# Optimization experiments

Measured on AMD Instinct MI355X. Metric: run time of the kernel, lower is better.

The kernel has to match this reference:

```python
import jax, jax.numpy as jnp
import numpy as np

L2_LAMDA = 0.001
RECONS_LAMDA = 0.2
LB_TH = 0.01
B, N, D = 32, 2048, 256


def setup_inputs() -> dict:
    key = jax.random.key(0)
    k1, k2, k3, k4 = jax.random.split(key, 4)
    cur = jax.random.normal(k1, (B, N, D), jnp.float32)
    pre = jax.random.normal(k2, (B, N, D), jnp.float32)
    lim_r = float(np.sqrt(6.0 / (D + D)))  # xavier_uniform bound
    r_proj = jax.random.uniform(k3, (D, D), jnp.float32, -lim_r, lim_r)
    lim_i = float(np.sqrt(6.0 / (N + N)))
    incidence_m = jax.random.uniform(k4, (N, N), jnp.float32, -lim_i, lim_i)
    return {"cur": cur, "pre": pre, "r_proj": r_proj, "incidence_m": incidence_m}


def reference(cur, pre, r_proj, incidence_m):
    # torch forward detaches cur/pre
    cur = jax.lax.stop_gradient(cur)
    pre = jax.lax.stop_gradient(pre)
    # clamp(min=lb_th) then zero where not (> lb_th)  ==  keep original where > lb_th else 0
    W = jnp.where(incidence_m > LB_TH, incidence_m, 0.0)          # (N, N)
    proj = jnp.einsum('bnd,de->bne', cur, r_proj)                 # (B, N, D)
    neigh = jnp.einsum('nm,bmd->bnd', W, pre)                     # (B, N, D)
    recon_err = jnp.sqrt(jnp.sum((proj - neigh) ** 2, axis=-1))   # (B, N)
    # torch: max(sum(abs(row[None,:]), dim=0)) == max-abs of the masked row
    l1 = jnp.max(jnp.abs(W), axis=1)                              # (N,)
    l2 = jnp.sqrt(jnp.sum(W ** 2, axis=1))                        # (N,)
    per_node = recon_err * RECONS_LAMDA + l1[None, :] + L2_LAMDA * l2[None, :]
    loss = jnp.sum(per_node, axis=1, keepdims=True)               # (B, 1)
    return loss, incidence_m
```

## Files before the change

### kernel.cpp

```cpp
#include <hip/hip_runtime.h>


typedef __attribute__((ext_vector_type(8))) short bf16x8;
typedef __attribute__((ext_vector_type(8))) unsigned short ushort8;
typedef __attribute__((ext_vector_type(16))) float f32x16;

__device__ __forceinline__ unsigned short f2bf(float f) {
    union { float f; unsigned u; } x; x.f = f;
    unsigned r = x.u + 0x7fffu + ((x.u >> 16) & 1u);
    return (unsigned short)(r >> 16);
}

#define GLL16(g, l)                                                         \
    __builtin_amdgcn_global_load_lds(                                       \
        (const __attribute__((address_space(1))) void*)(g),                 \
        (__attribute__((address_space(3))) void*)(l), 16, 0, 0)

__device__ __forceinline__ void transpose_64x64(
    const float* __restrict__ src, unsigned short* __restrict__ dst,
    int R, int C, int r0, int c0, unsigned short* __restrict__ tile) {
    const int t = threadIdx.x;
    const int fr = t >> 4, fc = (t & 15) * 4;
#pragma unroll
    for (int it = 0; it < 4; ++it) {
        int m = fr + it * 16;
        float4 v = *(const float4*)(src + (size_t)(r0 + m) * C + c0 + fc);
        tile[(fc + 0) * 68 + m] = f2bf(v.x);
        tile[(fc + 1) * 68 + m] = f2bf(v.y);
        tile[(fc + 2) * 68 + m] = f2bf(v.z);
        tile[(fc + 3) * 68 + m] = f2bf(v.w);
    }
    __syncthreads();
    const int d = t >> 2, m0 = (t & 3) * 16;
    unsigned short v[16];
#pragma unroll
    for (int j = 0; j < 4; ++j)
        *(ushort4*)(v + j * 4) = *(const ushort4*)(tile + d * 68 + m0 + j * 4);
    unsigned short* dp = dst + (size_t)(c0 + d) * R + r0 + m0;
    ushort8 p0, p1;
#pragma unroll
    for (int j = 0; j < 8; ++j) { p0[j] = v[j]; p1[j] = v[8 + j]; }
    *(ushort8*)(dp) = p0;
    *(ushort8*)(dp + 8) = p1;
}

__global__ __launch_bounds__(256) void prep_inc(
    const float* __restrict__ inc, float* __restrict__ out_inc,
    unsigned short* __restrict__ Wneg, float* __restrict__ crow) {
    __shared__ float smax[4], ssum[4];
    const int row = blockIdx.x;
    const int t = threadIdx.x;
    const float4* src = (const float4*)(inc + (size_t)row * 2048);
    float4* dst = (float4*)(out_inc + (size_t)row * 2048);
    ushort4* wp = (ushort4*)(Wneg + (size_t)row * 2048);
    float lmax = 0.f, ss = 0.f;
#pragma unroll
    for (int it = 0; it < 2; ++it) {
        int i = it * 256 + t;
        float4 v = src[i];
        dst[i] = v;
        float w0 = v.x > 0.01f ? v.x : 0.f;
        float w1 = v.y > 0.01f ? v.y : 0.f;
        float w2 = v.z > 0.01f ? v.z : 0.f;
        float w3 = v.w > 0.01f ? v.w : 0.f;
        ushort4 p;
        p.x = f2bf(-w0); p.y = f2bf(-w1); p.z = f2bf(-w2); p.w = f2bf(-w3);
        wp[i] = p;
        lmax = fmaxf(lmax, fmaxf(fmaxf(w0, w1), fmaxf(w2, w3)));
        ss += w0 * w0 + w1 * w1 + w2 * w2 + w3 * w3;
    }
#pragma unroll
    for (int off = 32; off; off >>= 1) {
        lmax = fmaxf(lmax, __shfl_down(lmax, off));
        ss += __shfl_down(ss, off);
    }
    int wv = t >> 6, ln = t & 63;
    if (ln == 0) { smax[wv] = lmax; ssum[wv] = ss; }
    __syncthreads();
    if (t == 0) {
        float m = fmaxf(fmaxf(smax[0], smax[1]), fmaxf(smax[2], smax[3]));
        float s = ssum[0] + ssum[1] + ssum[2] + ssum[3];
        crow[row] = m + 0.001f * sqrtf(s);
    }
}

__global__ __launch_bounds__(256) void prep_tr(
    const float* __restrict__ pre, unsigned short* __restrict__ preT,
    const float* __restrict__ r_proj, unsigned short* __restrict__ rprojT) {
    __shared__ unsigned short tile[64 * 68];
    const int bid = blockIdx.x;
    if (bid < 4096) {
        const int b = bid >> 7;
        const int mt = (bid & 127) >> 2;
        const int dt = bid & 3;
        transpose_64x64(pre + (size_t)b * 524288, preT + (size_t)b * 524288,
                        2048, 256, mt * 64, dt * 64, tile);
    } else {
        const int tt = bid - 4096;
        transpose_64x64(r_proj, rprojT, 256, 256, (tt >> 2) * 64, (tt & 3) * 64,
                        tile);
    }
}

__global__ __launch_bounds__(1024) void gemm_diff(
    const unsigned short* __restrict__ Wneg,
    const float* __restrict__ cur,
    const unsigned short* __restrict__ preT,
    const unsigned short* __restrict__ rprojT,
    float* __restrict__ Ssq)
{
    const int n0 = blockIdx.x * 256;
    const int b  = blockIdx.y;

    __shared__ unsigned short Al[2 * 256 * 64];
    __shared__ unsigned short Bl[2 * 256 * 64];
    __shared__ float ssq[256];

    const int tid  = threadIdx.x;
    const int w    = tid >> 6;
    const int lane = tid & 63;
    const int l32  = lane & 31;
    const int half = lane >> 5;
    const int wm   = w >> 2;
    const int wn   = w & 3;
    const int w8   = w * 8;
    const int grow  = lane >> 3;
    const int gbyte = ((lane & 7) ^ grow) * 16;
    const int sw    = (l32 & 7) * 8;

    if (tid < 256) ssq[tid] = 0.f;

    f32x16 acc[2][2] = {};

    const float*          curB = cur  + (size_t)b * 2048 * 256;
    const unsigned short* preB = preT + (size_t)b * 256 * 2048;
    const unsigned short* An   = Wneg + (size_t)n0 * 2048;

#define STAGE_TILE(AP, BP, K0)                                                 \
    {                                                                          \
        _Pragma("unroll") for (int pass = 0; pass < 2; ++pass) {               \
            const int rowb = pass * 128 + w8;                                  \
            GLL16((const char*)(An + (size_t)(rowb + grow) * 2048 + (K0)) + gbyte, \
                  (char*)(AP) + rowb * 128);                                   \
        }                                                                      \
        _Pragma("unroll") for (int pass = 0; pass < 2; ++pass) {               \
            const int rowb = pass * 128 + w8;                                  \
            GLL16((const char*)(preB + (size_t)(rowb + grow) * 2048 + (K0)) + gbyte, \
                  (char*)(BP) + rowb * 128);                                   \
        }                                                                      \
    }

#define KS_LOOP(Ac, Bc)                                                        \
    _Pragma("unroll") for (int ks = 0; ks < 4; ++ks) {                         \
        const int ck = (ks * 2 + half) * 8;                                    \
        bf16x8 af[2], bfr[2];                                                  \
        _Pragma("unroll") for (int mi = 0; mi < 2; ++mi)                       \
            af[mi] = *(const bf16x8*)((Ac) + (wm * 64 + mi * 32 + l32) * 64 +  \
                                      (ck ^ sw));                              \
        _Pragma("unroll") for (int ni = 0; ni < 2; ++ni)                       \
            bfr[ni] = *(const bf16x8*)((Bc) + (wn * 64 + ni * 32 + l32) * 64 + \
                                       (ck ^ sw));                             \
        _Pragma("unroll") for (int mi = 0; mi < 2; ++mi)                       \
        _Pragma("unroll") for (int ni = 0; ni < 2; ++ni)                       \
            acc[mi][ni] = __builtin_amdgcn_mfma_f32_32x32x16_bf16(             \
                af[mi], bfr[ni], acc[mi][ni], 0, 0, 0);                        \
    }

    STAGE_TILE(Al, Bl, 0);

    for (int t = 0; t < 32; ++t) {
        unsigned short* Ac = Al + (t & 1) * 16384;
        unsigned short* Bc = Bl + (t & 1) * 16384;
        unsigned short* Anx = Al + ((t & 1) ^ 1) * 16384;
        unsigned short* Bnx = Bl + ((t & 1) ^ 1) * 16384;

        asm volatile("s_waitcnt vmcnt(0)" ::: "memory");
        asm volatile("s_barrier" ::: "memory");
        if (t < 31) { STAGE_TILE(Anx, Bnx, (t + 1) * 64); }
        KS_LOOP(Ac, Bc)
    }

    for (int kt = 32; kt < 36; ++kt) {
        __syncthreads();
        const int kk = (kt - 32) * 64;
        const int row = tid >> 2;
        const int q   = tid & 3;
#pragma unroll
        for (int i = 0; i < 4; ++i) {
            const int k4 = q * 4 + i;
            float4 v = *(const float4*)(curB + (size_t)(n0 + row) * 256 + kk + k4 * 4);
            ushort4 p;
            p.x = f2bf(v.x); p.y = f2bf(v.y); p.z = f2bf(v.z); p.w = f2bf(v.w);
            const int pos = ((k4 >> 1) ^ (row & 7)) * 8 + (k4 & 1) * 4;
            *(ushort4*)(Al + row * 64 + pos) = p;
        }
#pragma unroll
        for (int pass = 0; pass < 2; ++pass) {
            const int rowb = pass * 128 + w8;
            GLL16((const char*)(rprojT + (size_t)(rowb + grow) * 256 + kk) + gbyte,
                  (char*)Bl + rowb * 128);
        }
        __syncthreads();
        KS_LOOP(Al, Bl)
    }
    __syncthreads();

#pragma unroll
    for (int mi = 0; mi < 2; ++mi)
#pragma unroll
        for (int reg = 0; reg < 16; ++reg) {
            float s = 0.f;
#pragma unroll
            for (int ni = 0; ni < 2; ++ni) {
                float v = acc[mi][ni][reg];
                s += v * v;
            }
            s += __shfl_xor(s, 1);
            s += __shfl_xor(s, 2);
            s += __shfl_xor(s, 4);
            s += __shfl_xor(s, 8);
            s += __shfl_xor(s, 16);
            if (l32 == 0) {
                const int row = wm * 64 + mi * 32 +
                                (reg & 3) + 8 * (reg >> 2) + 4 * half;
                atomicAdd(&ssq[row], s);
            }
        }
    __syncthreads();
    if (tid < 256)
        Ssq[(size_t)b * 2048 + n0 + tid] = sqrtf(ssq[tid]);
}

__global__ void finalize(const float* __restrict__ Ssq,
                         const float* __restrict__ crow,
                         float* __restrict__ out) {
    const int b = blockIdx.x;
    float s1 = 0.f, s2 = 0.f;
    for (int i = threadIdx.x; i < 2048; i += 256) {
        s1 += Ssq[(size_t)b * 2048 + i];
        s2 += crow[i];
    }
#pragma unroll
    for (int off = 32; off; off >>= 1) {
        s1 += __shfl_down(s1, off);
        s2 += __shfl_down(s2, off);
    }
    __shared__ float sm1[4], sm2[4];
    int wv = threadIdx.x >> 6, ln = threadIdx.x & 63;
    if (ln == 0) { sm1[wv] = s1; sm2[wv] = s2; }
    __syncthreads();
    if (threadIdx.x == 0)
        out[b] = 0.2f * (sm1[0] + sm1[1] + sm1[2] + sm1[3])
               + (sm2[0] + sm2[1] + sm2[2] + sm2[3]);
}

extern "C" void kernel_launch(void* const* d_in, const int* in_sizes, int n_in,
                              void* d_out, int out_size, void* d_ws, size_t ws_size,
                              hipStream_t stream) {
    const float* cur    = (const float*)d_in[0];
    const float* pre    = (const float*)d_in[1];
    const float* r_proj = (const float*)d_in[2];
    const float* inc    = (const float*)d_in[3];
    float* out = (float*)d_out;

    char* ws = (char*)d_ws;
    unsigned short* Wneg   = (unsigned short*)(ws + 0);
    unsigned short* preT   = (unsigned short*)(ws + 8388608);
    unsigned short* rprojT = (unsigned short*)(ws + 41943040);
    float*          Sbuf   = (float*)(ws + 42074112);
    float*          crow   = (float*)(ws + 42336256);

    prep_inc<<<2048, 256, 0, stream>>>(inc, out + 32, Wneg, crow);
    prep_tr<<<4112, 256, 0, stream>>>(pre, preT, r_proj, rprojT);
    gemm_diff<<<dim3(8, 32), 1024, 0, stream>>>(Wneg, cur, preT, rprojT, Sbuf);
    finalize<<<32, 256, 0, stream>>>(Sbuf, crow, out);
}
```

Measured before the change: 254.6 us.

## Pre-convert cur to bf16 and use 4-stage K32 async pipeline in gemm

Moves the fp32-to-bf16 conversion of cur into the prep kernel so the projection phase of the GEMM can use the same async global-to-LDS loads as the main phase. The GEMM loop is restructured into a uniform 72-step pipeline with 32-wide K tiles and a 4-deep LDS ring buffer, prefetching three tiles ahead using partial vmcnt waits instead of a full drain each step. This aims to hide memory latency and remove the synchronous tail loop, at the cost of an extra 32 MB write/read of cur in bf16 and more barriers per K.

```diff
diff --git a/kernel.cpp b/kernel.cpp
--- a/kernel.cpp
+++ b/kernel.cpp
@@ -86,25 +86,37 @@
 
 __global__ __launch_bounds__(256) void prep_tr(
     const float* __restrict__ pre, unsigned short* __restrict__ preT,
-    const float* __restrict__ r_proj, unsigned short* __restrict__ rprojT) {
+    const float* __restrict__ r_proj, unsigned short* __restrict__ rprojT,
+    const float* __restrict__ cur, unsigned short* __restrict__ curbf) {
     __shared__ unsigned short tile[64 * 68];
     const int bid = blockIdx.x;
+    const int t = threadIdx.x;
     if (bid < 4096) {
         const int b = bid >> 7;
         const int mt = (bid & 127) >> 2;
         const int dt = bid & 3;
         transpose_64x64(pre + (size_t)b * 524288, preT + (size_t)b * 524288,
                         2048, 256, mt * 64, dt * 64, tile);
-    } else {
+    } else if (bid < 4112) {
         const int tt = bid - 4096;
         transpose_64x64(r_proj, rprojT, 256, 256, (tt >> 2) * 64, (tt & 3) * 64,
                         tile);
+    } else {
+        const size_t base = (size_t)(bid - 4112) * 8192;
+#pragma unroll
+        for (int i = 0; i < 8; ++i) {
+            size_t idx = base + (size_t)(i * 256 + t) * 4;
+            float4 v = *(const float4*)(cur + idx);
+            ushort4 p;
+            p.x = f2bf(v.x); p.y = f2bf(v.y); p.z = f2bf(v.z); p.w = f2bf(v.w);
+            *(ushort4*)(curbf + idx) = p;
+        }
     }
 }
 
 __global__ __launch_bounds__(1024) void gemm_diff(
     const unsigned short* __restrict__ Wneg,
-    const float* __restrict__ cur,
+    const unsigned short* __restrict__ curbf,
     const unsigned short* __restrict__ preT,
     const unsigned short* __restrict__ rprojT,
     float* __restrict__ Ssq)
@@ -112,8 +124,8 @@
     const int n0 = blockIdx.x * 256;
     const int b  = blockIdx.y;
 
-    __shared__ unsigned short Al[2 * 256 * 64];
-    __shared__ unsigned short Bl[2 * 256 * 64];
+    __shared__ unsigned short Ab[4 * 256 * 32];
+    __shared__ unsigned short Bb[4 * 256 * 32];
     __shared__ float ssq[256];
 
     const int tid  = threadIdx.x;
@@ -123,85 +135,65 @@
     const int half = lane >> 5;
     const int wm   = w >> 2;
     const int wn   = w & 3;
-    const int w8   = w * 8;
-    const int grow  = lane >> 3;
-    const int gbyte = ((lane & 7) ^ grow) * 16;
-    const int sw    = (l32 & 7) * 8;
+    const int w16  = w * 16;
+    const int srow  = lane >> 2;
+    const int sbyte = ((lane & 3) ^ ((lane >> 3) & 3)) * 16;
+    const int q2    = (l32 >> 1) & 3;
 
     if (tid < 256) ssq[tid] = 0.f;
 
     f32x16 acc[2][2] = {};
 
-    const float*          curB = cur  + (size_t)b * 2048 * 256;
+    const unsigned short* curA = curbf + (size_t)b * 2048 * 256 + (size_t)n0 * 256;
     const unsigned short* preB = preT + (size_t)b * 256 * 2048;
     const unsigned short* An   = Wneg + (size_t)n0 * 2048;
 
-#define STAGE_TILE(AP, BP, K0)                                                 \
+#define STAGEPAIR(T, AB, AS, BB, BS, KK)                                       \
     {                                                                          \
-        _Pragma("unroll") for (int pass = 0; pass < 2; ++pass) {               \
-            const int rowb = pass * 128 + w8;                                  \
-            GLL16((const char*)(An + (size_t)(rowb + grow) * 2048 + (K0)) + gbyte, \
-                  (char*)(AP) + rowb * 128);                                   \
-        }                                                                      \
-        _Pragma("unroll") for (int pass = 0; pass < 2; ++pass) {               \
-            const int rowb = pass * 128 + w8;                                  \
-            GLL16((const char*)(preB + (size_t)(rowb + grow) * 2048 + (K0)) + gbyte, \
-                  (char*)(BP) + rowb * 128);                                   \
-        }                                                                      \
-    }
-
-#define KS_LOOP(Ac, Bc)                                                        \
-    _Pragma("unroll") for (int ks = 0; ks < 4; ++ks) {                         \
-        const int ck = (ks * 2 + half) * 8;                                    \
-        bf16x8 af[2], bfr[2];                                                  \
-        _Pragma("unroll") for (int mi = 0; mi < 2; ++mi)                       \
-            af[mi] = *(const bf16x8*)((Ac) + (wm * 64 + mi * 32 + l32) * 64 +  \
-                                      (ck ^ sw));                              \
-        _Pragma("unroll") for (int ni = 0; ni < 2; ++ni)                       \
-            bfr[ni] = *(const bf16x8*)((Bc) + (wn * 64 + ni * 32 + l32) * 64 + \
-                                       (ck ^ sw));                             \
-        _Pragma("unroll") for (int mi = 0; mi < 2; ++mi)                       \
-        _Pragma("unroll") for (int ni = 0; ni < 2; ++ni)                       \
-            acc[mi][ni] = __builtin_amdgcn_mfma_f32_32x32x16_bf16(             \
-                af[mi], bfr[ni], acc[mi][ni], 0, 0, 0);                        \
-    }
-
-    STAGE_TILE(Al, Bl, 0);
-
-    for (int t = 0; t < 32; ++t) {
-        unsigned short* Ac = Al + (t & 1) * 16384;
-        unsigned short* Bc = Bl + (t & 1) * 16384;
-        unsigned short* Anx = Al + ((t & 1) ^ 1) * 16384;
-        unsigned short* Bnx = Bl + ((t & 1) ^ 1) * 16384;
-
-        asm volatile("s_waitcnt vmcnt(0)" ::: "memory");
+        GLL16((const char*)((AB) + (size_t)(w16 + srow) * (AS) + (KK)) + sbyte,\
+              (char*)Ab + ((T) & 3) * 16384 + w * 1024);                       \
+        GLL16((const char*)((BB) + (size_t)(w16 + srow) * (BS) + (KK)) + sbyte,\
+              (char*)Bb + ((T) & 3) * 16384 + w * 1024);                       \
+    }
+
+    STAGEPAIR(0, An, 2048, preB, 2048, 0);
+    STAGEPAIR(1, An, 2048, preB, 2048, 32);
+    STAGEPAIR(2, An, 2048, preB, 2048, 64);
+
+    for (int t = 0; t < 72; ++t) {
+        if (t < 70)      asm volatile("s_waitcnt vmcnt(4)" ::: "memory");
+        else if (t == 70) asm volatile("s_waitcnt vmcnt(2)" ::: "memory");
+        else              asm volatile("s_waitcnt vmcnt(0)" ::: "memory");
         asm volatile("s_barrier" ::: "memory");
-        if (t < 31) { STAGE_TILE(Anx, Bnx, (t + 1) * 64); }
-        KS_LOOP(Ac, Bc)
-    }
-
-    for (int kt = 32; kt < 36; ++kt) {
-        __syncthreads();
-        const int kk = (kt - 32) * 64;
-        const int row = tid >> 2;
-        const int q   = tid & 3;
-#pragma unroll
-        for (int i = 0; i < 4; ++i) {
-            const int k4 = q * 4 + i;
-            float4 v = *(const float4*)(curB + (size_t)(n0 + row) * 256 + kk + k4 * 4);
-            ushort4 p;
-            p.x = f2bf(v.x); p.y = f2bf(v.y); p.z = f2bf(v.z); p.w = f2bf(v.w);
-            const int pos = ((k4 >> 1) ^ (row & 7)) * 8 + (k4 & 1) * 4;
-            *(ushort4*)(Al + row * 64 + pos) = p;
-        }
-#pragma unroll
-        for (int pass = 0; pass < 2; ++pass) {
-            const int rowb = pass * 128 + w8;
-            GLL16((const char*)(rprojT + (size_t)(rowb + grow) * 256 + kk) + gbyte,
-                  (char*)Bl + rowb * 128);
-        }
-        __syncthreads();
-        KS_LOOP(Al, Bl)
+
+        if (t < 69) {
+            const int t3 = t + 3;
+            const unsigned short *aB, *bB;
+            int aS, bS, kk;
+            if (t3 < 64) { aB = An;   aS = 2048; bB = preB;   bS = 2048; kk = t3 * 32; }
+            else         { aB = curA; aS = 256;  bB = rprojT; bS = 256;  kk = (t3 - 64) * 32; }
+            STAGEPAIR(t3, aB, aS, bB, bS, kk);
+        }
+
+        const unsigned short* Ac = Ab + (t & 3) * 8192;
+        const unsigned short* Bc = Bb + (t & 3) * 8192;
+#pragma unroll
+        for (int ks = 0; ks < 2; ++ks) {
+            const int co = (((ks << 1) + half) ^ q2) << 3;
+            bf16x8 af[2], bfr[2];
+#pragma unroll
+            for (int mi = 0; mi < 2; ++mi)
+                af[mi] = *(const bf16x8*)(Ac + (wm * 64 + mi * 32 + l32) * 32 + co);
+#pragma unroll
+            for (int ni = 0; ni < 2; ++ni)
+                bfr[ni] = *(const bf16x8*)(Bc + (wn * 64 + ni * 32 + l32) * 32 + co);
+#pragma unroll
+            for (int mi = 0; mi < 2; ++mi)
+#pragma unroll
+                for (int ni = 0; ni < 2; ++ni)
+                    acc[mi][ni] = __builtin_amdgcn_mfma_f32_32x32x16_bf16(
+                        af[mi], bfr[ni], acc[mi][ni], 0, 0, 0);
+        }
     }
     __syncthreads();
 
@@ -269,9 +261,10 @@
     unsigned short* rprojT = (unsigned short*)(ws + 41943040);
     float*          Sbuf   = (float*)(ws + 42074112);
     float*          crow   = (float*)(ws + 42336256);
+    unsigned short* curbf  = (unsigned short*)(ws + 42344448);
 
     prep_inc<<<2048, 256, 0, stream>>>(inc, out + 32, Wneg, crow);
-    prep_tr<<<4112, 256, 0, stream>>>(pre, preT, r_proj, rprojT);
-    gemm_diff<<<dim3(8, 32), 1024, 0, stream>>>(Wneg, cur, preT, rprojT, Sbuf);
+    prep_tr<<<6160, 256, 0, stream>>>(pre, preT, r_proj, rprojT, cur, curbf);
+    gemm_diff<<<dim3(8, 32), 1024, 0, stream>>>(Wneg, curbf, preT, rprojT, Sbuf);
     finalize<<<32, 256, 0, stream>>>(Sbuf, crow, out);
 }
```

Measured after the change: 265.6 us. 4.3% more time.
